# Performance work log

Measured on AMD Instinct MI355X. Metric: run time of the kernel, lower is better.

## Reference

```python
import jax, jax.numpy as jnp
import numpy as np

DIM = 1024
HEADS = 16
THS = 0.5  # deterministic threshold gating (forward called with ths=0.5)
C = float(np.e) * float(np.sqrt(1.0 / DIM))  # MaskedLinear init constant


def _pm_c(key, shape):
    # weights drawn from {-c, +c}, as in MaskedLinear 'mask' mode
    return jnp.where(jax.random.bernoulli(key, 0.5, shape), C, -C).astype(jnp.float32)


def setup_inputs() -> dict:
    key = jax.random.key(0)
    ks = jax.random.split(key, 7)
    b, n = 2, 2048
    return {
        "x": jax.random.normal(ks[0], (b, n, DIM), jnp.float32),
        "qkv_weight": _pm_c(ks[1], (3 * DIM, DIM)),
        "qkv_weight_mask": jax.random.normal(ks[2], (3 * DIM, DIM), jnp.float32),
        "out_weight": _pm_c(ks[3], (DIM, DIM)),
        "out_weight_mask": jax.random.normal(ks[4], (DIM, DIM), jnp.float32),
        "out_bias": _pm_c(ks[5], (DIM,)),
        "out_bias_mask": jax.random.normal(ks[6], (DIM,), jnp.float32),
    }


def reference(x, qkv_weight, qkv_weight_mask, out_weight, out_weight_mask,
              out_bias, out_bias_mask):
    b, n, _ = x.shape
    h, d = HEADS, DIM // HEADS
    dt = x.dtype

    # MaskedLinear (no bias): gate = 1[sigmoid(mask) > ths]
    g_qkv = (jax.nn.sigmoid(qkv_weight_mask) > THS).astype(dt)
    qkv = jnp.einsum('bnk,ok->bno', x, g_qkv * qkv_weight)  # [b, n, 3*dim]

    # rearrange 'b n (qkv h d) -> qkv b h n d'
    qkv = qkv.reshape(b, n, 3, h, d)
    q, k, v = (jnp.transpose(qkv[:, :, i], (0, 2, 1, 3)) for i in range(3))

    scale = DIM ** (-0.5)  # NOTE: full dim, matches source
    dots = jnp.einsum('bhid,bhjd->bhij', q, k) * scale  # [b, h, n, n]
    attn = jax.nn.softmax(dots, axis=-1)
    out = jnp.einsum('bhij,bhjd->bhid', attn, v)  # [b, h, n, d]
    out = jnp.transpose(out, (0, 2, 1, 3)).reshape(b, n, h * d)

    # MaskedLinear with bias
    g_w = (jax.nn.sigmoid(out_weight_mask) > THS).astype(dt)
    g_b = (jax.nn.sigmoid(out_bias_mask) > THS).astype(dt)
    out = jnp.einsum('bnk,ok->bno', out, g_w * out_weight) + g_b * out_bias
    # dropout: eval mode -> identity
    return out
```

## Files before the change

kernel.cpp:

```cpp
#include <hip/hip_runtime.h>

#define HEADS 16
#define DH 64
#define SEQ 2048
#define MROWS 4096
#define KDIM 1024
#define N3 3072

#define C_D (2.718281828459045 * 0.03125)
#define C_F ((float)C_D)
#define QSCALE ((float)(C_D * C_D / 32.0))

typedef __attribute__((ext_vector_type(8))) short bf16x8;
typedef __attribute__((ext_vector_type(4))) short s16x4;
typedef __attribute__((ext_vector_type(4))) float f32x4;
#define MFMA16 __builtin_amdgcn_mfma_f32_16x16x32_bf16

__device__ __forceinline__ unsigned short f2bf(float f) {
  unsigned int u = __float_as_uint(f);
  unsigned int r = u + 0x7FFFu + ((u >> 16) & 1u);
  return (unsigned short)(r >> 16);
}
__device__ __forceinline__ float bf2f(unsigned short h) {
  return __uint_as_float(((unsigned int)h) << 16);
}
__device__ __forceinline__ unsigned int split2u(float v) {
  const unsigned short hh = f2bf(v);
  const unsigned short ll = f2bf(v - bf2f(hh));
  return (unsigned int)hh | ((unsigned int)ll << 16);
}

__global__ __launch_bounds__(256) void sign_gate(const float* __restrict__ w,
                                                 const float* __restrict__ m,
                                                 unsigned short* __restrict__ s,
                                                 int n4) {
  const int i = blockIdx.x * 256 + threadIdx.x;
  if (i >= n4) return;
  const float4 wv = ((const float4*)w)[i];
  const float4 mv = ((const float4*)m)[i];
  s16x4 r;
  r[0] = (mv.x > 0.f) ? (wv.x > 0.f ? (short)0x3F80 : (short)0xBF80) : (short)0;
  r[1] = (mv.y > 0.f) ? (wv.y > 0.f ? (short)0x3F80 : (short)0xBF80) : (short)0;
  r[2] = (mv.z > 0.f) ? (wv.z > 0.f ? (short)0x3F80 : (short)0xBF80) : (short)0;
  r[3] = (mv.w > 0.f) ? (wv.w > 0.f ? (short)0x3F80 : (short)0xBF80) : (short)0;
  ((s16x4*)s)[i] = r;
}

template <int MODE>
__global__ __launch_bounds__(256) void gemm_mfma(
    const float* __restrict__ Af, const unsigned int* __restrict__ Apk,
    const unsigned short* __restrict__ Bsgn, const float* __restrict__ bias,
    const float* __restrict__ bias_m, unsigned int* __restrict__ qpk,
    unsigned short* __restrict__ khg, unsigned short* __restrict__ klg,
    unsigned short* __restrict__ vthg, unsigned short* __restrict__ vtlg,
    float* __restrict__ oo, int M, int N, int K) {
  __shared__ unsigned short Ah[128 * 40];
  __shared__ unsigned short Al[128 * 40];
  __shared__ unsigned short Bt[128 * 40];
  const int tid = threadIdx.x;
  const int l = tid & 63;
  const int w = tid >> 6;
  const int lr = l & 15, lg = l >> 4;
  const int wr = w >> 1, wc = w & 1;
  const int bm = blockIdx.y * 128, bn = blockIdx.x * 128;

  f32x4 acc[4][4];
#pragma unroll
  for (int i = 0; i < 4; ++i)
#pragma unroll
    for (int j = 0; j < 4; ++j)
#pragma unroll
      for (int r = 0; r < 4; ++r) acc[i][j][r] = 0.f;

  for (int k0 = 0; k0 < K; k0 += 32) {
    __syncthreads();
#pragma unroll
    for (int p = 0; p < 4; ++p) {
      const int ch = tid + p * 256;
      const int r = ch >> 3, c = ch & 7;
      s16x4 hv, lv;
      if (MODE == 0) {
        const float4 f = *(const float4*)&Af[(size_t)(bm + r) * K + k0 + c * 4];
        const unsigned int p0 = split2u(f.x), p1 = split2u(f.y),
                           p2 = split2u(f.z), p3 = split2u(f.w);
        hv[0] = (short)(p0 & 0xFFFFu); lv[0] = (short)(p0 >> 16);
        hv[1] = (short)(p1 & 0xFFFFu); lv[1] = (short)(p1 >> 16);
        hv[2] = (short)(p2 & 0xFFFFu); lv[2] = (short)(p2 >> 16);
        hv[3] = (short)(p3 & 0xFFFFu); lv[3] = (short)(p3 >> 16);
      } else {
        const uint4 u = *(const uint4*)&Apk[(size_t)(bm + r) * K + k0 + c * 4];
        hv[0] = (short)(u.x & 0xFFFFu); lv[0] = (short)(u.x >> 16);
        hv[1] = (short)(u.y & 0xFFFFu); lv[1] = (short)(u.y >> 16);
        hv[2] = (short)(u.z & 0xFFFFu); lv[2] = (short)(u.z >> 16);
        hv[3] = (short)(u.w & 0xFFFFu); lv[3] = (short)(u.w >> 16);
      }
      *(s16x4*)&Ah[r * 40 + c * 4] = hv;
      *(s16x4*)&Al[r * 40 + c * 4] = lv;
    }
#pragma unroll
    for (int p = 0; p < 2; ++p) {
      const int ch = tid + p * 256;
      const int r = ch >> 2, c = ch & 3;
      const uint4 u = *(const uint4*)&Bsgn[(size_t)(bn + r) * K + k0 + c * 8];
      *(uint4*)&Bt[r * 40 + c * 8] = u;
    }
    __syncthreads();

    bf16x8 af[4], alf[4], bfr[4];
#pragma unroll
    for (int i = 0; i < 4; ++i) {
      const int row = wr * 64 + i * 16 + lr;
      af[i] = *(const bf16x8*)&Ah[row * 40 + lg * 8];
      alf[i] = *(const bf16x8*)&Al[row * 40 + lg * 8];
    }
#pragma unroll
    for (int j = 0; j < 4; ++j)
      bfr[j] = *(const bf16x8*)&Bt[(wc * 64 + j * 16 + lr) * 40 + lg * 8];
#pragma unroll
    for (int i = 0; i < 4; ++i)
#pragma unroll
      for (int j = 0; j < 4; ++j) {
        acc[i][j] = MFMA16(af[i], bfr[j], acc[i][j], 0, 0, 0);
        acc[i][j] = MFMA16(alf[i], bfr[j], acc[i][j], 0, 0, 0);
      }
  }

  if (MODE == 0) {
    const int part = bn >> 10;
    const int rembase = bn & 1023;
#pragma unroll
    for (int i = 0; i < 4; ++i)
#pragma unroll
      for (int j = 0; j < 4; ++j) {
        const int gcol = rembase + wc * 64 + j * 16 + lr;
        const int h = gcol >> 6, d = gcol & 63;
#pragma unroll
        for (int r = 0; r < 4; ++r) {
          const int grow = bm + wr * 64 + i * 16 + lg * 4 + r;
          const int b = grow >> 11, n = grow & 2047;
          const int bh = b * HEADS + h;
          const float v = acc[i][j][r];
          if (part == 0) {
            qpk[((size_t)bh * SEQ + n) * DH + d] = split2u(v * QSCALE);
          } else if (part == 1) {
            const unsigned int u = split2u(v);
            const size_t idx = ((size_t)bh * SEQ + n) * DH + d;
            khg[idx] = (unsigned short)(u & 0xFFFFu);
            klg[idx] = (unsigned short)(u >> 16);
          } else {
            const unsigned int u = split2u(v * C_F);
            const size_t idx = ((size_t)bh * DH + d) * SEQ + n;
            vthg[idx] = (unsigned short)(u & 0xFFFFu);
            vtlg[idx] = (unsigned short)(u >> 16);
          }
        }
      }
  } else {
#pragma unroll
    for (int j = 0; j < 4; ++j) {
      const int gcol = bn + wc * 64 + j * 16 + lr;
      const float bg = (bias_m[gcol] > 0.f) ? bias[gcol] : 0.f;
#pragma unroll
      for (int i = 0; i < 4; ++i)
#pragma unroll
        for (int r = 0; r < 4; ++r) {
          const int grow = bm + wr * 64 + i * 16 + lg * 4 + r;
          oo[(size_t)grow * N + gcol] = acc[i][j][r] * C_F + bg;
        }
    }
  }
}

__global__ __launch_bounds__(256) void attn_mfma(
    const unsigned int* __restrict__ qpk, const unsigned short* __restrict__ khg,
    const unsigned short* __restrict__ klg,
    const unsigned short* __restrict__ vthg,
    const unsigned short* __restrict__ vtlg, unsigned int* __restrict__ aopk) {
  __shared__ unsigned short Kh[64 * 72];
  __shared__ unsigned short Kl[64 * 72];
  __shared__ unsigned short Vh[64 * 72];
  __shared__ unsigned short Vl[64 * 72];

  const int tid = threadIdx.x;
  const int l = tid & 63;
  const int w = tid >> 6;
  const int lr = l & 15, lg = l >> 4;
  const int qt = blockIdx.x;
  const int bh = blockIdx.y;

  bf16x8 qh[2], ql[2];
  const int q0 = qt * 64 + w * 16;
  const unsigned int* qrow = &qpk[((size_t)bh * SEQ + q0 + lr) * DH];
#pragma unroll
  for (int s = 0; s < 2; ++s) {
    const uint4 u0 = *(const uint4*)&qrow[s * 32 + lg * 8];
    const uint4 u1 = *(const uint4*)&qrow[s * 32 + lg * 8 + 4];
    bf16x8 h, lo;
    h[0] = (short)(u0.x & 0xFFFFu); lo[0] = (short)(u0.x >> 16);
    h[1] = (short)(u0.y & 0xFFFFu); lo[1] = (short)(u0.y >> 16);
    h[2] = (short)(u0.z & 0xFFFFu); lo[2] = (short)(u0.z >> 16);
    h[3] = (short)(u0.w & 0xFFFFu); lo[3] = (short)(u0.w >> 16);
    h[4] = (short)(u1.x & 0xFFFFu); lo[4] = (short)(u1.x >> 16);
    h[5] = (short)(u1.y & 0xFFFFu); lo[5] = (short)(u1.y >> 16);
    h[6] = (short)(u1.z & 0xFFFFu); lo[6] = (short)(u1.z >> 16);
    h[7] = (short)(u1.w & 0xFFFFu); lo[7] = (short)(u1.w >> 16);
    qh[s] = h;
    ql[s] = lo;
  }

  f32x4 oacc[4];
  float m_i[4], l_i[4];
#pragma unroll
  for (int dt = 0; dt < 4; ++dt)
#pragma unroll
    for (int r = 0; r < 4; ++r) oacc[dt][r] = 0.f;
#pragma unroll
  for (int r = 0; r < 4; ++r) {
    m_i[r] = -1e30f;
    l_i[r] = 0.f;
  }

  for (int kt = 0; kt < SEQ / 64; ++kt) {
    __syncthreads();
#pragma unroll
    for (int p = 0; p < 2; ++p) {
      const int ch = tid + p * 256;
      const int r = ch >> 3, c = ch & 7;
      const size_t kidx = ((size_t)bh * SEQ + kt * 64 + r) * DH + c * 8;
      const size_t vidx = ((size_t)bh * DH + r) * SEQ + kt * 64 + c * 8;
      *(uint4*)&Kh[r * 72 + c * 8] = *(const uint4*)&khg[kidx];
      *(uint4*)&Kl[r * 72 + c * 8] = *(const uint4*)&klg[kidx];
      *(uint4*)&Vh[r * 72 + c * 8] = *(const uint4*)&vthg[vidx];
      *(uint4*)&Vl[r * 72 + c * 8] = *(const uint4*)&vtlg[vidx];
    }
    __syncthreads();

    f32x4 sacc[4];
#pragma unroll
    for (int ct = 0; ct < 4; ++ct)
#pragma unroll
      for (int r = 0; r < 4; ++r) sacc[ct][r] = 0.f;
#pragma unroll
    for (int ct = 0; ct < 4; ++ct)
#pragma unroll
      for (int s = 0; s < 2; ++s) {
        const int off = (ct * 16 + lr) * 72 + s * 32 + lg * 8;
        const bf16x8 kh = *(const bf16x8*)&Kh[off];
        const bf16x8 kl = *(const bf16x8*)&Kl[off];
        sacc[ct] = MFMA16(qh[s], kh, sacc[ct], 0, 0, 0);
        sacc[ct] = MFMA16(qh[s], kl, sacc[ct], 0, 0, 0);
        sacc[ct] = MFMA16(ql[s], kh, sacc[ct], 0, 0, 0);
      }

    float ps[4][4], alpha[4];
#pragma unroll
    for (int r = 0; r < 4; ++r) {
      float mx = fmaxf(fmaxf(sacc[0][r], sacc[1][r]),
                       fmaxf(sacc[2][r], sacc[3][r]));
#pragma unroll
      for (int off = 1; off < 16; off <<= 1) mx = fmaxf(mx, __shfl_xor(mx, off));
      const float mn = fmaxf(m_i[r], mx);
      alpha[r] = __expf(m_i[r] - mn);
      float rs = 0.f;
#pragma unroll
      for (int ct = 0; ct < 4; ++ct) {
        ps[ct][r] = __expf(sacc[ct][r] - mn);
        rs += ps[ct][r];
      }
#pragma unroll
      for (int off = 1; off < 16; off <<= 1) rs += __shfl_xor(rs, off);
      l_i[r] = l_i[r] * alpha[r] + rs;
      m_i[r] = mn;
    }

#pragma unroll
    for (int dt = 0; dt < 4; ++dt)
#pragma unroll
      for (int r = 0; r < 4; ++r) oacc[dt][r] *= alpha[r];

    __syncthreads();

#pragma unroll
    for (int ct = 0; ct < 4; ++ct)
#pragma unroll
      for (int r = 0; r < 4; ++r) {
        const unsigned short h = f2bf(ps[ct][r]);
        const int rowoff = (w * 16 + lg * 4 + r) * 72 + ct * 16 + lr;
        Kh[rowoff] = h;
        Kl[rowoff] = f2bf(ps[ct][r] - bf2f(h));
      }

#pragma unroll
    for (int s = 0; s < 2; ++s) {
      const int poff = (w * 16 + lr) * 72 + s * 32 + lg * 8;
      const bf16x8 ph = *(const bf16x8*)&Kh[poff];
      const bf16x8 pl = *(const bf16x8*)&Kl[poff];
#pragma unroll
      for (int dt = 0; dt < 4; ++dt) {
        const int off = (dt * 16 + lr) * 72 + s * 32 + lg * 8;
        const bf16x8 vh = *(const bf16x8*)&Vh[off];
        const bf16x8 vl = *(const bf16x8*)&Vl[off];
        oacc[dt] = MFMA16(ph, vh, oacc[dt], 0, 0, 0);
        oacc[dt] = MFMA16(ph, vl, oacc[dt], 0, 0, 0);
        oacc[dt] = MFMA16(pl, vh, oacc[dt], 0, 0, 0);
      }
    }
  }

  const int b = bh >> 4, hh = bh & 15;
#pragma unroll
  for (int r = 0; r < 4; ++r) {
    const float inv = 1.f / l_i[r];
    const int n = qt * 64 + w * 16 + lg * 4 + r;
#pragma unroll
    for (int dt = 0; dt < 4; ++dt)
      aopk[((size_t)(b * SEQ + n)) * KDIM + hh * DH + dt * 16 + lr] =
          split2u(oacc[dt][r] * inv);
  }
}

extern "C" void kernel_launch(void* const* d_in, const int* in_sizes, int n_in,
                              void* d_out, int out_size, void* d_ws,
                              size_t ws_size, hipStream_t stream) {
  const float* x = (const float*)d_in[0];
  const float* qkvw = (const float*)d_in[1];
  const float* qkvm = (const float*)d_in[2];
  const float* outw = (const float*)d_in[3];
  const float* outm = (const float*)d_in[4];
  const float* ob = (const float*)d_in[5];
  const float* obm = (const float*)d_in[6];
  float* out = (float*)d_out;

  char* base = (char*)d_ws;
  unsigned int* qpk = (unsigned int*)base;
  unsigned short* khg = (unsigned short*)(base + (16u << 20));
  unsigned short* klg = (unsigned short*)(base + (24u << 20));
  unsigned short* vthg = (unsigned short*)(base + (32u << 20));
  unsigned short* vtlg = (unsigned short*)(base + (40u << 20));
  unsigned int* aopk = (unsigned int*)(base + (48u << 20));
  unsigned short* sq = (unsigned short*)aopk;
  unsigned short* so = (unsigned short*)qpk;

  sign_gate<<<dim3(N3 * KDIM / 4 / 256), 256, 0, stream>>>(qkvw, qkvm, sq,
                                                           N3 * KDIM / 4);
  gemm_mfma<0><<<dim3(N3 / 128, MROWS / 128), 256, 0, stream>>>(
      x, nullptr, sq, nullptr, nullptr, qpk, khg, klg, vthg, vtlg, nullptr,
      MROWS, N3, KDIM);
  attn_mfma<<<dim3(SEQ / 64, 32), 256, 0, stream>>>(qpk, khg, klg, vthg, vtlg,
                                                    aopk);
  sign_gate<<<dim3(KDIM * KDIM / 4 / 256), 256, 0, stream>>>(outw, outm, so,
                                                             KDIM * KDIM / 4);
  gemm_mfma<1><<<dim3(KDIM / 128, MROWS / 128), 256, 0, stream>>>(
      nullptr, aopk, so, ob, obm, nullptr, nullptr, nullptr, nullptr, nullptr,
      out, MROWS, KDIM, KDIM);
}
```

Before: 413.1 us.

## Prefetch next K/V tile into registers and XOR-swizzle attention LDS layout

The attention kernel now loads the next K/V tile from global memory into registers while the current tile is being computed, then writes those registers to shared memory at the start of the next iteration. This hides global load latency behind the MFMA work. It also replaces the padded 72-element LDS rows with unpadded 64-element rows that use an XOR swizzle on the 8-element chunk index, which keeps bank conflicts low and shrinks shared memory. The cost is 8 extra uint4 registers per thread, which may reduce occupancy.

```diff
diff --git a/kernel.cpp b/kernel.cpp
--- a/kernel.cpp
+++ b/kernel.cpp
@@ -176,10 +176,10 @@
     const unsigned short* __restrict__ klg,
     const unsigned short* __restrict__ vthg,
     const unsigned short* __restrict__ vtlg, unsigned int* __restrict__ aopk) {
-  __shared__ unsigned short Kh[64 * 72];
-  __shared__ unsigned short Kl[64 * 72];
-  __shared__ unsigned short Vh[64 * 72];
-  __shared__ unsigned short Vl[64 * 72];
+  __shared__ unsigned short Kh[64 * 64];
+  __shared__ unsigned short Kl[64 * 64];
+  __shared__ unsigned short Vh[64 * 64];
+  __shared__ unsigned short Vl[64 * 64];
 
   const int tid = threadIdx.x;
   const int l = tid & 63;
@@ -208,6 +208,28 @@
     ql[s] = lo;
   }
 
+  const int sr0 = tid >> 3, sc = tid & 7;
+  const int sr1 = sr0 + 32;
+  const int so0 = sr0 * 64 + ((sc ^ (sr0 & 7)) << 3);
+  const int so1 = sr1 * 64 + ((sc ^ (sr1 & 7)) << 3);
+  uint4 rk0h, rk1h, rk0l, rk1l, rv0h, rv1h, rv0l, rv1l;
+
+#define LOAD_TILE(KT)                                                        \
+  do {                                                                       \
+    const size_t k0 = ((size_t)bh * SEQ + (KT)*64 + sr0) * DH + sc * 8;      \
+    const size_t k1 = ((size_t)bh * SEQ + (KT)*64 + sr1) * DH + sc * 8;      \
+    const size_t v0 = ((size_t)bh * DH + sr0) * SEQ + (KT)*64 + sc * 8;      \
+    const size_t v1 = ((size_t)bh * DH + sr1) * SEQ + (KT)*64 + sc * 8;      \
+    rk0h = *(const uint4*)&khg[k0];                                          \
+    rk1h = *(const uint4*)&khg[k1];                                          \
+    rk0l = *(const uint4*)&klg[k0];                                          \
+    rk1l = *(const uint4*)&klg[k1];                                          \
+    rv0h = *(const uint4*)&vthg[v0];                                         \
+    rv1h = *(const uint4*)&vthg[v1];                                         \
+    rv0l = *(const uint4*)&vtlg[v0];                                         \
+    rv1l = *(const uint4*)&vtlg[v1];                                         \
+  } while (0)
+
   f32x4 oacc[4];
   float m_i[4], l_i[4];
 #pragma unroll
@@ -220,19 +242,19 @@
     l_i[r] = 0.f;
   }
 
+  LOAD_TILE(0);
+
   for (int kt = 0; kt < SEQ / 64; ++kt) {
     __syncthreads();
-#pragma unroll
-    for (int p = 0; p < 2; ++p) {
-      const int ch = tid + p * 256;
-      const int r = ch >> 3, c = ch & 7;
-      const size_t kidx = ((size_t)bh * SEQ + kt * 64 + r) * DH + c * 8;
-      const size_t vidx = ((size_t)bh * DH + r) * SEQ + kt * 64 + c * 8;
-      *(uint4*)&Kh[r * 72 + c * 8] = *(const uint4*)&khg[kidx];
-      *(uint4*)&Kl[r * 72 + c * 8] = *(const uint4*)&klg[kidx];
-      *(uint4*)&Vh[r * 72 + c * 8] = *(const uint4*)&vthg[vidx];
-      *(uint4*)&Vl[r * 72 + c * 8] = *(const uint4*)&vtlg[vidx];
-    }
+    *(uint4*)&Kh[so0] = rk0h;
+    *(uint4*)&Kh[so1] = rk1h;
+    *(uint4*)&Kl[so0] = rk0l;
+    *(uint4*)&Kl[so1] = rk1l;
+    *(uint4*)&Vh[so0] = rv0h;
+    *(uint4*)&Vh[so1] = rv1h;
+    *(uint4*)&Vl[so0] = rv0l;
+    *(uint4*)&Vl[so1] = rv1l;
+    if (kt + 1 < SEQ / 64) LOAD_TILE(kt + 1);
     __syncthreads();
 
     f32x4 sacc[4];
@@ -244,7 +266,7 @@
     for (int ct = 0; ct < 4; ++ct)
 #pragma unroll
       for (int s = 0; s < 2; ++s) {
-        const int off = (ct * 16 + lr) * 72 + s * 32 + lg * 8;
+        const int off = (ct * 16 + lr) * 64 + (((s * 4 + lg) ^ (lr & 7)) << 3);
         const bf16x8 kh = *(const bf16x8*)&Kh[off];
         const bf16x8 kl = *(const bf16x8*)&Kl[off];
         sacc[ct] = MFMA16(qh[s], kh, sacc[ct], 0, 0, 0);
@@ -285,19 +307,22 @@
 #pragma unroll
       for (int r = 0; r < 4; ++r) {
         const unsigned short h = f2bf(ps[ct][r]);
-        const int rowoff = (w * 16 + lg * 4 + r) * 72 + ct * 16 + lr;
-        Kh[rowoff] = h;
-        Kl[rowoff] = f2bf(ps[ct][r] - bf2f(h));
+        const int qr = w * 16 + lg * 4 + r;
+        const int pchunk = ct * 2 + (lr >> 3);
+        const int pidx =
+            qr * 64 + ((pchunk ^ ((lg * 4 + r) & 7)) << 3) + (lr & 7);
+        Kh[pidx] = h;
+        Kl[pidx] = f2bf(ps[ct][r] - bf2f(h));
       }
 
 #pragma unroll
     for (int s = 0; s < 2; ++s) {
-      const int poff = (w * 16 + lr) * 72 + s * 32 + lg * 8;
+      const int poff = (w * 16 + lr) * 64 + (((s * 4 + lg) ^ (lr & 7)) << 3);
       const bf16x8 ph = *(const bf16x8*)&Kh[poff];
       const bf16x8 pl = *(const bf16x8*)&Kl[poff];
 #pragma unroll
       for (int dt = 0; dt < 4; ++dt) {
-        const int off = (dt * 16 + lr) * 72 + s * 32 + lg * 8;
+        const int off = (dt * 16 + lr) * 64 + (((s * 4 + lg) ^ (lr & 7)) << 3);
         const bf16x8 vh = *(const bf16x8*)&Vh[off];
         const bf16x8 vl = *(const bf16x8*)&Vl[off];
         oacc[dt] = MFMA16(ph, vh, oacc[dt], 0, 0, 0);
@@ -306,6 +331,7 @@
       }
     }
   }
+#undef LOAD_TILE
 
   const int b = bh >> 4, hh = bh & 15;
 #pragma unroll
```

Result: slower. 472.3 us (+14.3%).
